# Kernel tuning notes

Hardware: AMD Instinct MI355X
Metric: run time of the kernel (lower is better)

## Reference

```python
import jax, jax.numpy as jnp
import numpy as np

HID = 64

def setup_inputs() -> dict:
    key = jax.random.key(0)
    ks = jax.random.split(key, 32)
    Nc, Na, B = 65536, 8192, 128
    Ecc, Eca, Eac, Eaa = 1048576, 262144, 262144, 131072
    d = {}
    d['x_context'] = jax.random.normal(ks[0], (Nc, 2), jnp.float32)
    d['x_action'] = jax.random.normal(ks[1], (Na, 2), jnp.float32)
    d['timestep'] = jax.random.randint(ks[2], (B,), 0, 1000)
    d['batch_idx'] = jax.random.randint(ks[3], (Na,), 0, B)
    d['cc_src'] = jax.random.randint(ks[4], (Ecc,), 0, Nc)
    d['cc_dst'] = jax.random.randint(ks[5], (Ecc,), 0, Nc)
    d['ca_src'] = jax.random.randint(ks[6], (Eca,), 0, Nc)
    d['ca_dst'] = jax.random.randint(ks[7], (Eca,), 0, Na)
    d['ac_src'] = jax.random.randint(ks[8], (Eac,), 0, Na)
    d['ac_dst'] = jax.random.randint(ks[9], (Eac,), 0, Nc)
    d['aa_src'] = jax.random.randint(ks[10], (Eaa,), 0, Na)
    d['aa_dst'] = jax.random.randint(ks[11], (Eaa,), 0, Na)
    def w(k, shape, fan_in):
        return jax.random.normal(k, shape, jnp.float32) / np.sqrt(fan_in)
    # input embeddings
    d['W_ctx'] = w(ks[12], (2, HID), 2); d['b_ctx'] = jnp.zeros((HID,), jnp.float32)
    d['W_act'] = w(ks[13], (2, HID), 2); d['b_act'] = jnp.zeros((HID,), jnp.float32)
    # time MLP
    d['tW1'] = w(ks[14], (HID, 2 * HID), HID); d['tb1'] = jnp.zeros((2 * HID,), jnp.float32)
    d['tW2'] = w(ks[15], (2 * HID, HID), 2 * HID); d['tb2'] = jnp.zeros((HID,), jnp.float32)
    # 2 SAGE layers, 4 edge types each (stacked: [cc, ca, ac, aa])
    d['c1_Wl'] = w(ks[16], (4, HID, HID), HID); d['c1_bl'] = jnp.zeros((4, HID), jnp.float32)
    d['c1_Wr'] = w(ks[17], (4, HID, HID), HID)
    d['c2_Wl'] = w(ks[18], (4, HID, HID), HID); d['c2_bl'] = jnp.zeros((4, HID), jnp.float32)
    d['c2_Wr'] = w(ks[19], (4, HID, HID), HID)
    # noise predictor
    d['nW1'] = w(ks[20], (2 * HID, HID), 2 * HID); d['nb1'] = jnp.zeros((HID,), jnp.float32)
    d['nW2'] = w(ks[21], (HID, 2), HID); d['nb2'] = jnp.zeros((2,), jnp.float32)
    return d


def _sage(x_src, x_dst, src, dst, Wl, bl, Wr):
    # PyG SAGEConv: lin_l(mean of neighbor msgs) + lin_r(self)
    n_dst = x_dst.shape[0]
    s = jax.ops.segment_sum(x_src[src], dst, num_segments=n_dst)
    cnt = jax.ops.segment_sum(jnp.ones((src.shape[0], 1), x_src.dtype), dst, num_segments=n_dst)
    mean = s / jnp.maximum(cnt, 1.0)
    return mean @ Wl + bl + x_dst @ Wr


def reference(x_context, x_action, timestep, batch_idx, cc_src, cc_dst, ca_src, ca_dst, ac_src, ac_dst, aa_src, aa_dst, W_ctx, b_ctx, W_act, b_act, tW1, tb1, tW2, tb2, c1_Wl, c1_bl, c1_Wr, c2_Wl, c2_bl, c2_Wr, nW1, nb1, nW2, nb2):
    h_ctx = x_context @ W_ctx + b_ctx           # [Nc, H]
    h_act = x_action @ W_act + b_act            # [Na, H]
    # hetero SAGE layer 1 (aggr='sum' over edge types per dst node type)
    o_ctx = (_sage(h_ctx, h_ctx, cc_src, cc_dst, c1_Wl[0], c1_bl[0], c1_Wr[0])
             + _sage(h_act, h_ctx, ac_src, ac_dst, c1_Wl[2], c1_bl[2], c1_Wr[2]))
    o_act = (_sage(h_ctx, h_act, ca_src, ca_dst, c1_Wl[1], c1_bl[1], c1_Wr[1])
             + _sage(h_act, h_act, aa_src, aa_dst, c1_Wl[3], c1_bl[3], c1_Wr[3]))
    h_ctx, h_act = jax.nn.relu(o_ctx), jax.nn.relu(o_act)
    # hetero SAGE layer 2
    o_act = (_sage(h_ctx, h_act, ca_src, ca_dst, c2_Wl[1], c2_bl[1], c2_Wr[1])
             + _sage(h_act, h_act, aa_src, aa_dst, c2_Wl[3], c2_bl[3], c2_Wr[3]))
    action_features = o_act                      # [Na, H]
    # sinusoidal time embedding + MLP
    half = HID // 2
    freqs = jnp.exp(-jnp.log(10000.0) * jnp.arange(half, dtype=jnp.float32) / (half - 1))
    ang = timestep.astype(jnp.float32)[:, None] * freqs[None, :]
    temb = jnp.concatenate([jnp.sin(ang), jnp.cos(ang)], axis=-1)   # [B, H]
    temb = jax.nn.gelu(temb @ tW1 + tb1, approximate=False) @ tW2 + tb2
    # gather per-node time embedding, fuse, predict noise
    fused = jnp.concatenate([action_features, temb[batch_idx]], axis=-1)  # [Na, 2H]
    h = jax.nn.gelu(fused @ nW1 + nb1, approximate=False)
    return h @ nW2 + nb2                         # [Na, node_features]
```

## Files before the change

### kernel.cpp

```cpp
#include <hip/hip_runtime.h>
#include <math.h>

#define HID 64
#define SLOTS 8192
#define WCC 32
#define WAC 10
#define SCA 8
#define SAA 4
#define HCA 16
#define HAA 8
#define CAP_CA 112
#define CAP_AA 80

__device__ __forceinline__ float gelu_exact(float x) {
    return 0.5f * x * (1.0f + erff(x * 0.70710678118654752f));
}

__device__ __forceinline__ float bf2f(unsigned short u) {
    return __uint_as_float(((unsigned int)u) << 16);
}
__device__ __forceinline__ unsigned short f2bf(float x) {
    unsigned int b = __float_as_uint(x);
    b += 0x7FFFu + ((b >> 16) & 1u);
    return (unsigned short)(b >> 16);
}

#define FXS 32768.0f
#define FXB (1 << 19)

__device__ __forceinline__ unsigned long long pack_edge(float2 v) {
    unsigned int f0 = (unsigned int)(__float2int_rn(v.x * FXS) + FXB);
    unsigned int f1 = (unsigned int)(__float2int_rn(v.y * FXS) + FXB);
    return (1ULL << 52) | ((unsigned long long)f1 << 26) | f0;
}

__device__ __forceinline__ void decode_acc(unsigned long long A, float& s0, float& s1, float& c) {
    int cnt = (int)(A >> 52);
    long long f0 = (long long)(A & 0x3FFFFFFULL) - (long long)cnt * FXB;
    long long f1 = (long long)((A >> 26) & 0x3FFFFFFULL) - (long long)cnt * FXB;
    s0 = (float)f0 * (1.0f / FXS);
    s1 = (float)f1 * (1.0f / FXS);
    c = (float)cnt;
}

__global__ __launch_bounds__(1024) void k1_kernel(
    const float* __restrict__ W_ctx, const float* __restrict__ b_ctx,
    const float* __restrict__ W_act, const float* __restrict__ b_act,
    const float* __restrict__ c1_Wl, const float* __restrict__ c1_bl,
    const float* __restrict__ c1_Wr,
    const float* __restrict__ c2_Wr, const float* __restrict__ c2_bl,
    float* __restrict__ P,
    const int* __restrict__ timestep,
    const float* __restrict__ tW1, const float* __restrict__ tb1,
    const float* __restrict__ tW2, const float* __restrict__ tb2,
    float* __restrict__ temb, int B,
    const int* __restrict__ cc_src, const int* __restrict__ cc_dst,
    const float* __restrict__ x_ctx, unsigned long long* __restrict__ pcc,
    int Ecc, int perCC,
    const int* __restrict__ ac_src, const int* __restrict__ ac_dst,
    const float* __restrict__ x_act, unsigned long long* __restrict__ pac,
    int Eac, int perAC,
    const int* __restrict__ ca_src, const int* __restrict__ ca_dst, int Eca,
    const int* __restrict__ aa_src, const int* __restrict__ aa_dst, int Eaa,
    unsigned long long* __restrict__ pca, unsigned long long* __restrict__ paa,
    int* __restrict__ hca, int* __restrict__ haa,
    int Nc, int bCC, int bAC, int bXA, int bXB, int bHA, int bHB) {
    __shared__ unsigned long long slab[SLOTS];
    int blk = blockIdx.x;
    int tid = threadIdx.x;

    if (blk < 6) {
        int m = blk;
        const float* vw = (m == 0 || m == 1 || m == 4) ? W_ctx : W_act;
        const float* vb = (m == 0 || m == 1 || m == 4) ? b_ctx : b_act;
        const float* L1; const float* L2 = nullptr; int off;
        if (m == 0)      { L1 = c1_Wr;            L2 = c1_Wr + 2 * 4096; off = 0; }
        else if (m == 1) { L1 = c1_Wl;                                   off = 192; }
        else if (m == 2) { L1 = c1_Wl + 2 * 4096;                        off = 384; }
        else if (m == 3) { L1 = c1_Wr + 4096;     L2 = c1_Wr + 3 * 4096; off = 576; }
        else if (m == 4) { L1 = c1_Wl + 4096;                            off = 768; }
        else             { L1 = c1_Wl + 3 * 4096;                        off = 960; }
        int j = tid & 63, kc = tid >> 6;
        float a0 = 0.f, a1 = 0.f, cc = 0.f;
        #pragma unroll
        for (int kk = 0; kk < 4; kk++) {
            int k = kc * 4 + kk;
            float l = L1[k * 64 + j];
            if (L2) l += L2[k * 64 + j];
            a0 += vw[k] * l; a1 += vw[64 + k] * l; cc += vb[k] * l;
        }
        float* red = (float*)slab;
        red[(kc * 3 + 0) * 64 + j] = a0;
        red[(kc * 3 + 1) * 64 + j] = a1;
        red[(kc * 3 + 2) * 64 + j] = cc;
        __syncthreads();
        if (tid < 192) {
            int row = tid >> 6, jj = tid & 63;
            float s = 0.f;
            #pragma unroll
            for (int q = 0; q < 16; q++) s += red[(q * 3 + row) * 64 + jj];
            if (row == 2) {
                if (m == 0) s += c1_bl[jj] + c1_bl[128 + jj];
                if (m == 3) s += c1_bl[64 + jj] + c1_bl[192 + jj];
            }
            P[off + row * 64 + jj] = s;
        }
    } else if (blk == 6) {
        const float4* A4 = (const float4*)(c2_Wr + 4096);
        const float4* B4 = (const float4*)(c2_Wr + 3 * 4096);
        float4* O4 = (float4*)(P + 1152);
        float4 a = A4[tid], b = B4[tid];
        O4[tid] = make_float4(a.x + b.x, a.y + b.y, a.z + b.z, a.w + b.w);
        if (tid < 64) P[5248 + tid] = c2_bl[64 + tid] + c2_bl[192 + tid];
    } else if (blk < bCC) {
        float* fl = (float*)slab;
        int sub = tid >> 7;
        int t = tid & 127;
        int b = (blk - 7) * 8 + sub;
        bool vb = (b < B);
        float* e = fl + sub * 64;
        float* t1 = fl + 2048 + sub * 128;
        float ts = vb ? (float)timestep[b] : 0.f;
        if (t < 64) {
            int jj = t & 31;
            float f = expf(-9.210340371976184f * (float)jj / 31.0f);
            float ang = ts * f;
            e[t] = (t < 32) ? sinf(ang) : cosf(ang);
        }
        __syncthreads();
        {
            float a = tb1[t];
            #pragma unroll 8
            for (int k = 0; k < 64; k++) a += e[k] * tW1[k * 128 + t];
            t1[t] = gelu_exact(a);
        }
        __syncthreads();
        if (t < 64 && vb) {
            float a = tb2[t];
            #pragma unroll 8
            for (int k = 0; k < 128; k++) a += t1[k] * tW2[k * 64 + t];
            temb[b * 64 + t] = a;
        }
    } else if (blk < bAC) {
        int q = blk - bCC;
        int r = q / WCC, s = q % WCC;
        for (int k = tid; k < SLOTS; k += 1024) slab[k] = 0;
        __syncthreads();
        int lo = r * SLOTS;
        int e0 = s * perCC;
        int e1 = min(e0 + perCC, Ecc);
        const float2* xc2 = (const float2*)x_ctx;
        for (int e = e0 + tid * 4; e < e1; e += 4096) {
            int4 d4 = *(const int4*)(cc_dst + e);
            unsigned int o0 = (unsigned int)(d4.x - lo);
            unsigned int o1 = (unsigned int)(d4.y - lo);
            unsigned int o2 = (unsigned int)(d4.z - lo);
            unsigned int o3 = (unsigned int)(d4.w - lo);
            if ((o0 < SLOTS) | (o1 < SLOTS) | (o2 < SLOTS) | (o3 < SLOTS)) {
                int4 s4 = *(const int4*)(cc_src + e);
                if (o0 < SLOTS) atomicAdd(&slab[o0], pack_edge(xc2[s4.x]));
                if (o1 < SLOTS) atomicAdd(&slab[o1], pack_edge(xc2[s4.y]));
                if (o2 < SLOTS) atomicAdd(&slab[o2], pack_edge(xc2[s4.z]));
                if (o3 < SLOTS) atomicAdd(&slab[o3], pack_edge(xc2[s4.w]));
            }
        }
        __syncthreads();
        for (int k = tid; k < SLOTS; k += 1024)
            pcc[(size_t)s * Nc + lo + k] = slab[k];
    } else if (blk < bXA) {
        int q = blk - bAC;
        int r = q / WAC, s = q % WAC;
        for (int k = tid; k < SLOTS; k += 1024) slab[k] = 0;
        __syncthreads();
        int lo = r * SLOTS;
        int e0 = s * perAC;
        int e1 = min(e0 + perAC, Eac);
        const float2* xa2 = (const float2*)x_act;
        for (int e = e0 + tid * 4; e < e1; e += 4096) {
            int4 d4 = *(const int4*)(ac_dst + e);
            unsigned int o0 = (unsigned int)(d4.x - lo);
            unsigned int o1 = (unsigned int)(d4.y - lo);
            unsigned int o2 = (unsigned int)(d4.z - lo);
            unsigned int o3 = (unsigned int)(d4.w - lo);
            if ((o0 < SLOTS) | (o1 < SLOTS) | (o2 < SLOTS) | (o3 < SLOTS)) {
                int4 s4 = *(const int4*)(ac_src + e);
                if (o0 < SLOTS) atomicAdd(&slab[o0], pack_edge(xa2[s4.x]));
                if (o1 < SLOTS) atomicAdd(&slab[o1], pack_edge(xa2[s4.y]));
                if (o2 < SLOTS) atomicAdd(&slab[o2], pack_edge(xa2[s4.z]));
                if (o3 < SLOTS) atomicAdd(&slab[o3], pack_edge(xa2[s4.w]));
            }
        }
        __syncthreads();
        for (int k = tid; k < SLOTS; k += 1024)
            pac[(size_t)s * Nc + lo + k] = slab[k];
    } else if (blk < bXB) {
        int s = blk - bXA;
        for (int k = tid; k < SLOTS; k += 1024) slab[k] = 0;
        __syncthreads();
        int per = (Eca + SCA - 1) / SCA;
        int e0 = s * per, e1 = min(e0 + per, Eca);
        const float2* xc2 = (const float2*)x_ctx;
        for (int e = e0 + tid * 4; e < e1; e += 4096) {
            int4 d4 = *(const int4*)(ca_dst + e);
            int4 s4 = *(const int4*)(ca_src + e);
            atomicAdd(&slab[d4.x], pack_edge(xc2[s4.x]));
            atomicAdd(&slab[d4.y], pack_edge(xc2[s4.y]));
            atomicAdd(&slab[d4.z], pack_edge(xc2[s4.z]));
            atomicAdd(&slab[d4.w], pack_edge(xc2[s4.w]));
        }
        __syncthreads();
        for (int k = tid; k < SLOTS; k += 1024)
            pca[(size_t)s * SLOTS + k] = slab[k];
    } else if (blk < bHA) {
        int s = blk - bXB;
        for (int k = tid; k < SLOTS; k += 1024) slab[k] = 0;
        __syncthreads();
        int per = (Eaa + SAA - 1) / SAA;
        int e0 = s * per, e1 = min(e0 + per, Eaa);
        const float2* xa2 = (const float2*)x_act;
        for (int e = e0 + tid * 4; e < e1; e += 4096) {
            int4 d4 = *(const int4*)(aa_dst + e);
            int4 s4 = *(const int4*)(aa_src + e);
            atomicAdd(&slab[d4.x], pack_edge(xa2[s4.x]));
            atomicAdd(&slab[d4.y], pack_edge(xa2[s4.y]));
            atomicAdd(&slab[d4.z], pack_edge(xa2[s4.z]));
            atomicAdd(&slab[d4.w], pack_edge(xa2[s4.w]));
        }
        __syncthreads();
        for (int k = tid; k < SLOTS; k += 1024)
            paa[(size_t)s * SLOTS + k] = slab[k];
    } else if (blk < bHB) {
        int s = blk - bHA;
        int* hist = (int*)slab;
        for (int k = tid; k < SLOTS; k += 1024) hist[k] = 0;
        __syncthreads();
        int per = (Eca + HCA - 1) / HCA;
        int e0 = s * per, e1 = min(e0 + per, Eca);
        for (int e = e0 + tid * 4; e < e1; e += 4096) {
            int4 d4 = *(const int4*)(ca_dst + e);
            atomicAdd(&hist[d4.x], 1); atomicAdd(&hist[d4.y], 1);
            atomicAdd(&hist[d4.z], 1); atomicAdd(&hist[d4.w], 1);
        }
        __syncthreads();
        for (int k = tid; k < SLOTS; k += 1024) hca[s * SLOTS + k] = hist[k];
    } else {
        int s = blk - bHB;
        int* hist = (int*)slab;
        for (int k = tid; k < SLOTS; k += 1024) hist[k] = 0;
        __syncthreads();
        int per = (Eaa + HAA - 1) / HAA;
        int e0 = s * per, e1 = min(e0 + per, Eaa);
        for (int e = e0 + tid * 4; e < e1; e += 4096) {
            int4 d4 = *(const int4*)(aa_dst + e);
            atomicAdd(&hist[d4.x], 1); atomicAdd(&hist[d4.y], 1);
            atomicAdd(&hist[d4.z], 1); atomicAdd(&hist[d4.w], 1);
        }
        __syncthreads();
        for (int k = tid; k < SLOTS; k += 1024) haa[s * SLOTS + k] = hist[k];
    }
}

__global__ void k2_kernel(int* __restrict__ hca, int* __restrict__ haa,
                          int* __restrict__ cnt_ca, int* __restrict__ cnt_aa) {
    int d = blockIdx.x * 1024 + threadIdx.x;
    int run = 0;
    #pragma unroll
    for (int s = 0; s < HCA; s++) {
        int h = hca[s * SLOTS + d];
        hca[s * SLOTS + d] = run;
        run += h;
    }
    cnt_ca[d] = run;
    run = 0;
    #pragma unroll
    for (int s = 0; s < HAA; s++) {
        int h = haa[s * SLOTS + d];
        haa[s * SLOTS + d] = run;
        run += h;
    }
    cnt_aa[d] = run;
}

__global__ __launch_bounds__(1024) void k3_kernel(
    const int* __restrict__ ca_src, const int* __restrict__ ca_dst, int Eca,
    const int* __restrict__ aa_src, const int* __restrict__ aa_dst, int Eaa,
    const int* __restrict__ hca, const int* __restrict__ haa,
    int* __restrict__ csr_ca, int* __restrict__ csr_aa,
    const unsigned long long* __restrict__ pcc, const unsigned long long* __restrict__ pac,
    const unsigned long long* __restrict__ pca, const unsigned long long* __restrict__ paa,
    const float* __restrict__ x_ctx, const float* __restrict__ x_act,
    const float* __restrict__ P,
    unsigned short* __restrict__ hb_ctx, unsigned short* __restrict__ hb_act,
    int Nc, int Na, int bCTX, int bACT) {
    __shared__ int sh[SLOTS];
    int blk = blockIdx.x;
    int tid = threadIdx.x;

    if (blk < HCA) {
        int s = blk;
        for (int k = tid; k < SLOTS; k += 1024) sh[k] = hca[s * SLOTS + k];
        __syncthreads();
        int per = (Eca + HCA - 1) / HCA;
        int e0 = s * per, e1 = min(e0 + per, Eca);
        for (int e = e0 + tid * 4; e < e1; e += 4096) {
            int4 d4 = *(const int4*)(ca_dst + e);
            int4 s4 = *(const int4*)(ca_src + e);
            int p0 = atomicAdd(&sh[d4.x], 1);
            int p1 = atomicAdd(&sh[d4.y], 1);
            int p2 = atomicAdd(&sh[d4.z], 1);
            int p3 = atomicAdd(&sh[d4.w], 1);
            if (p0 < CAP_CA) csr_ca[d4.x * CAP_CA + p0] = s4.x;
            if (p1 < CAP_CA) csr_ca[d4.y * CAP_CA + p1] = s4.y;
            if (p2 < CAP_CA) csr_ca[d4.z * CAP_CA + p2] = s4.z;
            if (p3 < CAP_CA) csr_ca[d4.w * CAP_CA + p3] = s4.w;
        }
    } else if (blk < bCTX) {
        int s = blk - HCA;
        for (int k = tid; k < SLOTS; k += 1024) sh[k] = haa[s * SLOTS + k];
        __syncthreads();
        int per = (Eaa + HAA - 1) / HAA;
        int e0 = s * per, e1 = min(e0 + per, Eaa);
        for (int e = e0 + tid * 4; e < e1; e += 4096) {
            int4 d4 = *(const int4*)(aa_dst + e);
            int4 s4 = *(const int4*)(aa_src + e);
            int p0 = atomicAdd(&sh[d4.x], 1);
            int p1 = atomicAdd(&sh[d4.y], 1);
            int p2 = atomicAdd(&sh[d4.z], 1);
            int p3 = atomicAdd(&sh[d4.w], 1);
            if (p0 < CAP_AA) csr_aa[d4.x * CAP_AA + p0] = s4.x;
            if (p1 < CAP_AA) csr_aa[d4.y * CAP_AA + p1] = s4.y;
            if (p2 < CAP_AA) csr_aa[d4.z * CAP_AA + p2] = s4.z;
            if (p3 < CAP_AA) csr_aa[d4.w * CAP_AA + p3] = s4.w;
        }
    } else if (blk < bACT) {
        float (*nd)[8] = (float(*)[8])sh;
        int i = (blk - bCTX) * 1024 + tid;
        if (i < Nc) {
            unsigned long long A = 0, Bv = 0;
            #pragma unroll 8
            for (int s = 0; s < WCC; s++) A += pcc[(size_t)s * Nc + i];
            #pragma unroll
            for (int s = 0; s < WAC; s++) Bv += pac[(size_t)s * Nc + i];
            float s0, s1, cc, a0, a1, ca;
            decode_acc(A, s0, s1, cc);
            decode_acc(Bv, a0, a1, ca);
            float2 xv = ((const float2*)x_ctx)[i];
            float rcc = 1.f / fmaxf(cc, 1.f), rac = 1.f / fmaxf(ca, 1.f);
            nd[tid][0] = s0 * rcc; nd[tid][1] = s1 * rcc; nd[tid][2] = (cc > 0.f) ? 1.f : 0.f;
            nd[tid][3] = a0 * rac; nd[tid][4] = a1 * rac; nd[tid][5] = (ca > 0.f) ? 1.f : 0.f;
            nd[tid][6] = xv.x; nd[tid][7] = xv.y;
        }
        __syncthreads();
        int ns = tid >> 6, j = tid & 63;
        float p0 = P[j], p1 = P[64 + j], p2 = P[128 + j];
        float p3 = P[192 + j], p4 = P[256 + j], p5 = P[320 + j];
        float p6 = P[384 + j], p7 = P[448 + j], p8 = P[512 + j];
        for (int it = 0; it < 64; it++) {
            int ln = it * 16 + ns;
            int gi = (blk - bCTX) * 1024 + ln;
            if (gi >= Nc) break;
            float o = nd[ln][6] * p0 + nd[ln][7] * p1 + p2
                    + nd[ln][0] * p3 + nd[ln][1] * p4 + nd[ln][2] * p5
                    + nd[ln][3] * p6 + nd[ln][4] * p7 + nd[ln][5] * p8;
            hb_ctx[(size_t)gi * 64 + j] = f2bf(fmaxf(o, 0.f));
        }
    } else {
        float (*nd)[8] = (float(*)[8])sh;
        int i = (blk - bACT) * 1024 + tid;
        if (i < Na) {
            unsigned long long A = 0, Bv = 0;
            #pragma unroll
            for (int s = 0; s < SCA; s++) A += pca[(size_t)s * SLOTS + i];
            #pragma unroll
            for (int s = 0; s < SAA; s++) Bv += paa[(size_t)s * SLOTS + i];
            float s0, s1, cc, a0, a1, ca;
            decode_acc(A, s0, s1, cc);
            decode_acc(Bv, a0, a1, ca);
            float2 xv = ((const float2*)x_act)[i];
            float rca = 1.f / fmaxf(cc, 1.f), raa = 1.f / fmaxf(ca, 1.f);
            nd[tid][0] = s0 * rca; nd[tid][1] = s1 * rca; nd[tid][2] = (cc > 0.f) ? 1.f : 0.f;
            nd[tid][3] = a0 * raa; nd[tid][4] = a1 * raa; nd[tid][5] = (ca > 0.f) ? 1.f : 0.f;
            nd[tid][6] = xv.x; nd[tid][7] = xv.y;
        }
        __syncthreads();
        int ns = tid >> 6, j = tid & 63;
        float p0 = P[576 + j], p1 = P[640 + j], p2 = P[704 + j];
        float p3 = P[768 + j], p4 = P[832 + j], p5 = P[896 + j];
        float p6 = P[960 + j], p7 = P[1024 + j], p8 = P[1088 + j];
        for (int it = 0; it < 64; it++) {
            int ln = it * 16 + ns;
            int gi = (blk - bACT) * 1024 + ln;
            if (gi >= Na) break;
            float o = nd[ln][6] * p0 + nd[ln][7] * p1 + p2
                    + nd[ln][0] * p3 + nd[ln][1] * p4 + nd[ln][2] * p5
                    + nd[ln][3] * p6 + nd[ln][4] * p7 + nd[ln][5] * p8;
            hb_act[(size_t)gi * 64 + j] = f2bf(fmaxf(o, 0.f));
        }
    }
}

__global__ void k4_kernel(const unsigned short* __restrict__ hb_ctx,
                          const unsigned short* __restrict__ hb_act,
                          const int* __restrict__ cnt_ca, const int* __restrict__ csr_ca,
                          const int* __restrict__ cnt_aa, const int* __restrict__ csr_aa,
                          const float* __restrict__ c2_Wl, const float* __restrict__ P,
                          const float* __restrict__ temb, const int* __restrict__ batch_idx,
                          const float* __restrict__ nW1, const float* __restrict__ nb1,
                          const float* __restrict__ nW2, const float* __restrict__ nb2,
                          float* __restrict__ out, int N) {
    int n = threadIdx.x >> 6;
    int l = threadIdx.x & 63;
    int half = l >> 5;
    int c2 = l & 31;
    int i = blockIdx.x * 4 + n;
    bool act = (i < N);
    __shared__ float smca[4][64], smaa[4][64], shr[4][64], sfused[4][128], sh1[4][64];

    const unsigned int* hc32 = (const unsigned int*)hb_ctx;
    const unsigned int* ha32 = (const unsigned int*)hb_act;

    if (act) {
        int m = cnt_ca[i], mi = min(m, CAP_CA);
        int b = i * CAP_CA;
        float s0 = 0.f, s1 = 0.f;
        #pragma unroll 4
        for (int k = half; k < mi; k += 2) {
            unsigned int w = hc32[(size_t)csr_ca[b + k] * 32 + c2];
            s0 += bf2f((unsigned short)(w & 0xFFFFu));
            s1 += bf2f((unsigned short)(w >> 16));
        }
        s0 += __shfl_xor(s0, 32);
        s1 += __shfl_xor(s1, 32);
        float rm = 1.f / fmaxf((float)m, 1.f);
        if (half == 0) { smca[n][c2 * 2] = s0 * rm; smca[n][c2 * 2 + 1] = s1 * rm; }

        m = cnt_aa[i]; mi = min(m, CAP_AA);
        b = i * CAP_AA;
        s0 = 0.f; s1 = 0.f;
        #pragma unroll 4
        for (int k = half; k < mi; k += 2) {
            unsigned int w = ha32[(size_t)csr_aa[b + k] * 32 + c2];
            s0 += bf2f((unsigned short)(w & 0xFFFFu));
            s1 += bf2f((unsigned short)(w >> 16));
        }
        s0 += __shfl_xor(s0, 32);
        s1 += __shfl_xor(s1, 32);
        rm = 1.f / fmaxf((float)m, 1.f);
        if (half == 0) { smaa[n][c2 * 2] = s0 * rm; smaa[n][c2 * 2 + 1] = s1 * rm; }

        shr[n][l] = bf2f(hb_act[(size_t)i * 64 + l]);
    }
    __syncthreads();

    if (act) {
        const float* Wl1  = c2_Wl + 4096;
        const float* Wl3  = c2_Wl + 3 * 4096;
        const float* Wr2s = P + 1152;
        float o = P[5248 + l];
        #pragma unroll 8
        for (int k = 0; k < 64; k++) {
            o += smca[n][k] * Wl1[k * 64 + l]
               + smaa[n][k] * Wl3[k * 64 + l]
               + shr[n][k]  * Wr2s[k * 64 + l];
        }
        sfused[n][l] = o;
        sfused[n][64 + l] = temb[(size_t)batch_idx[i] * 64 + l];
    }
    __syncthreads();

    if (act) {
        float h = nb1[l];
        #pragma unroll 8
        for (int k = 0; k < 128; k++) h += sfused[n][k] * nW1[k * 64 + l];
        sh1[n][l] = gelu_exact(h);
    }
    __syncthreads();

    if (act && l < 2) {
        float v = nb2[l];
        #pragma unroll 8
        for (int k = 0; k < 64; k++) v += sh1[n][k] * nW2[k * 2 + l];
        out[(size_t)i * 2 + l] = v;
    }
}

extern "C" void kernel_launch(void* const* d_in, const int* in_sizes, int n_in,
                              void* d_out, int out_size, void* d_ws, size_t ws_size,
                              hipStream_t stream) {
    const float* x_context = (const float*)d_in[0];
    const float* x_action  = (const float*)d_in[1];
    const int*   timestep  = (const int*)d_in[2];
    const int*   batch_idx = (const int*)d_in[3];
    const int*   cc_src = (const int*)d_in[4];
    const int*   cc_dst = (const int*)d_in[5];
    const int*   ca_src = (const int*)d_in[6];
    const int*   ca_dst = (const int*)d_in[7];
    const int*   ac_src = (const int*)d_in[8];
    const int*   ac_dst = (const int*)d_in[9];
    const int*   aa_src = (const int*)d_in[10];
    const int*   aa_dst = (const int*)d_in[11];
    const float* W_ctx = (const float*)d_in[12];
    const float* b_ctx = (const float*)d_in[13];
    const float* W_act = (const float*)d_in[14];
    const float* b_act = (const float*)d_in[15];
    const float* tW1 = (const float*)d_in[16];
    const float* tb1 = (const float*)d_in[17];
    const float* tW2 = (const float*)d_in[18];
    const float* tb2 = (const float*)d_in[19];
    const float* c1_Wl = (const float*)d_in[20];
    const float* c1_bl = (const float*)d_in[21];
    const float* c1_Wr = (const float*)d_in[22];
    const float* c2_Wl = (const float*)d_in[23];
    const float* c2_bl = (const float*)d_in[24];
    const float* c2_Wr = (const float*)d_in[25];
    const float* nW1 = (const float*)d_in[26];
    const float* nb1 = (const float*)d_in[27];
    const float* nW2 = (const float*)d_in[28];
    const float* nb2 = (const float*)d_in[29];
    float* out = (float*)d_out;

    const int Nc  = in_sizes[0] / 2;
    const int Na  = in_sizes[1] / 2;
    const int B   = in_sizes[2];
    const int Ecc = in_sizes[4];
    const int Eca = in_sizes[6];
    const int Eac = in_sizes[8];
    const int Eaa = in_sizes[10];

    char* ws = (char*)d_ws;
    size_t o = 0;
    unsigned long long* pcc = (unsigned long long*)(ws + o); o += (size_t)WCC * Nc * 8;
    unsigned long long* pac = (unsigned long long*)(ws + o); o += (size_t)WAC * Nc * 8;
    unsigned long long* pca = (unsigned long long*)(ws + o); o += (size_t)SCA * SLOTS * 8;
    unsigned long long* paa = (unsigned long long*)(ws + o); o += (size_t)SAA * SLOTS * 8;
    int* hca    = (int*)(ws + o); o += (size_t)HCA * SLOTS * 4;
    int* haa    = (int*)(ws + o); o += (size_t)HAA * SLOTS * 4;
    int* cnt_ca = (int*)(ws + o); o += (size_t)Na * 4;
    int* cnt_aa = (int*)(ws + o); o += (size_t)Na * 4;
    int* csr_ca = (int*)(ws + o); o += (size_t)Na * CAP_CA * 4;
    int* csr_aa = (int*)(ws + o); o += (size_t)Na * CAP_AA * 4;
    float* P    = (float*)(ws + o); o += 8192 * 4;
    float* temb = (float*)(ws + o); o += (size_t)B * 64 * 4;
    unsigned short* hb_ctx = (unsigned short*)(ws + o); o += (size_t)Nc * 64 * 2;
    unsigned short* hb_act = (unsigned short*)(ws + o); o += (size_t)Na * 64 * 2;
    if (o > ws_size) return;

    const int RNG = (Nc + SLOTS - 1) / SLOTS;
    const int nT  = (B + 7) / 8;
    const int bCC = 7 + nT;
    const int bAC = bCC + RNG * WCC;
    const int bXA = bAC + RNG * WAC;
    const int bXB = bXA + SCA;
    const int bHA = bXB + SAA;
    const int bHB = bHA + HCA;
    const int G1  = bHB + HAA;
    const int perCC = (((Ecc + WCC - 1) / WCC) + 3) & ~3;
    const int perAC = (((Eac + WAC - 1) / WAC) + 3) & ~3;

    k1_kernel<<<G1, 1024, 0, stream>>>(
        W_ctx, b_ctx, W_act, b_act, c1_Wl, c1_bl, c1_Wr, c2_Wr, c2_bl, P,
        timestep, tW1, tb1, tW2, tb2, temb, B,
        cc_src, cc_dst, x_context, pcc, Ecc, perCC,
        ac_src, ac_dst, x_action, pac, Eac, perAC,
        ca_src, ca_dst, Eca, aa_src, aa_dst, Eaa,
        pca, paa, hca, haa,
        Nc, bCC, bAC, bXA, bXB, bHA, bHB);

    k2_kernel<<<(Na + 1023) / 1024, 1024, 0, stream>>>(hca, haa, cnt_ca, cnt_aa);

    const int bCTX = HCA + HAA;
    const int GctxB = (Nc + 1023) / 1024;
    const int bACT = bCTX + GctxB;
    const int GactB = (Na + 1023) / 1024;
    k3_kernel<<<bACT + GactB, 1024, 0, stream>>>(
        ca_src, ca_dst, Eca, aa_src, aa_dst, Eaa,
        hca, haa, csr_ca, csr_aa,
        pcc, pac, pca, paa,
        x_context, x_action, P, hb_ctx, hb_act,
        Nc, Na, bCTX, bACT);

    k4_kernel<<<(Na + 3) / 4, 256, 0, stream>>>(
        hb_ctx, hb_act, cnt_ca, csr_ca, cnt_aa, csr_aa,
        c2_Wl, P, temb, batch_idx, nW1, nb1, nW2, nb2, out, Na);
}
```

Before: 100.4 us.

## Split fused multi-role kernels into separate per-stage launches

Breaks the block-index-dispatched kernel k1 into four kernels: weight precompute plus time MLP, cc scatter, ac scatter, and ca/aa scatter plus histograms. It likewise splits k3 into a CSR-fill kernel and a node-update kernel. Each kernel now declares only the shared memory it needs, so the small time-MLP blocks no longer reserve a 64KB slab. Independent stages that used to run concurrently inside one grid now run one after another on the stream, which adds launch gaps and removes that overlap.

After: 143.4 us. 1.43x slower.

```diff
diff --git a/kernel.cpp b/kernel.cpp
--- a/kernel.cpp
+++ b/kernel.cpp
@@ -43,7 +43,7 @@
     c = (float)cnt;
 }
 
-__global__ __launch_bounds__(1024) void k1_kernel(
+__global__ __launch_bounds__(1024) void kA_kernel(
     const float* __restrict__ W_ctx, const float* __restrict__ b_ctx,
     const float* __restrict__ W_act, const float* __restrict__ b_act,
     const float* __restrict__ c1_Wl, const float* __restrict__ c1_bl,
@@ -53,19 +53,8 @@
     const int* __restrict__ timestep,
     const float* __restrict__ tW1, const float* __restrict__ tb1,
     const float* __restrict__ tW2, const float* __restrict__ tb2,
-    float* __restrict__ temb, int B,
-    const int* __restrict__ cc_src, const int* __restrict__ cc_dst,
-    const float* __restrict__ x_ctx, unsigned long long* __restrict__ pcc,
-    int Ecc, int perCC,
-    const int* __restrict__ ac_src, const int* __restrict__ ac_dst,
-    const float* __restrict__ x_act, unsigned long long* __restrict__ pac,
-    int Eac, int perAC,
-    const int* __restrict__ ca_src, const int* __restrict__ ca_dst, int Eca,
-    const int* __restrict__ aa_src, const int* __restrict__ aa_dst, int Eaa,
-    unsigned long long* __restrict__ pca, unsigned long long* __restrict__ paa,
-    int* __restrict__ hca, int* __restrict__ haa,
-    int Nc, int bCC, int bAC, int bXA, int bXB, int bHA, int bHB) {
-    __shared__ unsigned long long slab[SLOTS];
+    float* __restrict__ temb, int B) {
+    __shared__ float fl[3072];
     int blk = blockIdx.x;
     int tid = threadIdx.x;
 
@@ -89,16 +78,15 @@
             if (L2) l += L2[k * 64 + j];
             a0 += vw[k] * l; a1 += vw[64 + k] * l; cc += vb[k] * l;
         }
-        float* red = (float*)slab;
-        red[(kc * 3 + 0) * 64 + j] = a0;
-        red[(kc * 3 + 1) * 64 + j] = a1;
-        red[(kc * 3 + 2) * 64 + j] = cc;
+        fl[(kc * 3 + 0) * 64 + j] = a0;
+        fl[(kc * 3 + 1) * 64 + j] = a1;
+        fl[(kc * 3 + 2) * 64 + j] = cc;
         __syncthreads();
         if (tid < 192) {
             int row = tid >> 6, jj = tid & 63;
             float s = 0.f;
             #pragma unroll
-            for (int q = 0; q < 16; q++) s += red[(q * 3 + row) * 64 + jj];
+            for (int q = 0; q < 16; q++) s += fl[(q * 3 + row) * 64 + jj];
             if (row == 2) {
                 if (m == 0) s += c1_bl[jj] + c1_bl[128 + jj];
                 if (m == 3) s += c1_bl[64 + jj] + c1_bl[192 + jj];
@@ -112,14 +100,13 @@
         float4 a = A4[tid], b = B4[tid];
         O4[tid] = make_float4(a.x + b.x, a.y + b.y, a.z + b.z, a.w + b.w);
         if (tid < 64) P[5248 + tid] = c2_bl[64 + tid] + c2_bl[192 + tid];
-    } else if (blk < bCC) {
-        float* fl = (float*)slab;
+    } else {
         int sub = tid >> 7;
         int t = tid & 127;
         int b = (blk - 7) * 8 + sub;
         bool vb = (b < B);
         float* e = fl + sub * 64;
-        float* t1 = fl + 2048 + sub * 128;
+        float* t1 = fl + 2048 + ((sub & 7) * 128);
         float ts = vb ? (float)timestep[b] : 0.f;
         if (t < 64) {
             int jj = t & 31;
@@ -132,69 +119,94 @@
             float a = tb1[t];
             #pragma unroll 8
             for (int k = 0; k < 64; k++) a += e[k] * tW1[k * 128 + t];
-            t1[t] = gelu_exact(a);
+            fl[1024 + sub * 128 + t] = gelu_exact(a);
         }
         __syncthreads();
         if (t < 64 && vb) {
+            const float* t1p = fl + 1024 + sub * 128;
             float a = tb2[t];
             #pragma unroll 8
-            for (int k = 0; k < 128; k++) a += t1[k] * tW2[k * 64 + t];
+            for (int k = 0; k < 128; k++) a += t1p[k] * tW2[k * 64 + t];
             temb[b * 64 + t] = a;
         }
-    } else if (blk < bAC) {
-        int q = blk - bCC;
-        int r = q / WCC, s = q % WCC;
-        for (int k = tid; k < SLOTS; k += 1024) slab[k] = 0;
-        __syncthreads();
-        int lo = r * SLOTS;
-        int e0 = s * perCC;
-        int e1 = min(e0 + perCC, Ecc);
-        const float2* xc2 = (const float2*)x_ctx;
-        for (int e = e0 + tid * 4; e < e1; e += 4096) {
-            int4 d4 = *(const int4*)(cc_dst + e);
-            unsigned int o0 = (unsigned int)(d4.x - lo);
-            unsigned int o1 = (unsigned int)(d4.y - lo);
-            unsigned int o2 = (unsigned int)(d4.z - lo);
-            unsigned int o3 = (unsigned int)(d4.w - lo);
-            if ((o0 < SLOTS) | (o1 < SLOTS) | (o2 < SLOTS) | (o3 < SLOTS)) {
-                int4 s4 = *(const int4*)(cc_src + e);
-                if (o0 < SLOTS) atomicAdd(&slab[o0], pack_edge(xc2[s4.x]));
-                if (o1 < SLOTS) atomicAdd(&slab[o1], pack_edge(xc2[s4.y]));
-                if (o2 < SLOTS) atomicAdd(&slab[o2], pack_edge(xc2[s4.z]));
-                if (o3 < SLOTS) atomicAdd(&slab[o3], pack_edge(xc2[s4.w]));
-            }
-        }
-        __syncthreads();
-        for (int k = tid; k < SLOTS; k += 1024)
-            pcc[(size_t)s * Nc + lo + k] = slab[k];
-    } else if (blk < bXA) {
-        int q = blk - bAC;
-        int r = q / WAC, s = q % WAC;
-        for (int k = tid; k < SLOTS; k += 1024) slab[k] = 0;
-        __syncthreads();
-        int lo = r * SLOTS;
-        int e0 = s * perAC;
-        int e1 = min(e0 + perAC, Eac);
-        const float2* xa2 = (const float2*)x_act;
-        for (int e = e0 + tid * 4; e < e1; e += 4096) {
-            int4 d4 = *(const int4*)(ac_dst + e);
-            unsigned int o0 = (unsigned int)(d4.x - lo);
-            unsigned int o1 = (unsigned int)(d4.y - lo);
-            unsigned int o2 = (unsigned int)(d4.z - lo);
-            unsigned int o3 = (unsigned int)(d4.w - lo);
-            if ((o0 < SLOTS) | (o1 < SLOTS) | (o2 < SLOTS) | (o3 < SLOTS)) {
-                int4 s4 = *(const int4*)(ac_src + e);
-                if (o0 < SLOTS) atomicAdd(&slab[o0], pack_edge(xa2[s4.x]));
-                if (o1 < SLOTS) atomicAdd(&slab[o1], pack_edge(xa2[s4.y]));
-                if (o2 < SLOTS) atomicAdd(&slab[o2], pack_edge(xa2[s4.z]));
-                if (o3 < SLOTS) atomicAdd(&slab[o3], pack_edge(xa2[s4.w]));
-            }
-        }
-        __syncthreads();
-        for (int k = tid; k < SLOTS; k += 1024)
-            pac[(size_t)s * Nc + lo + k] = slab[k];
-    } else if (blk < bXB) {
-        int s = blk - bXA;
+    }
+}
+
+__global__ __launch_bounds__(1024) void kB_kernel(
+    const int* __restrict__ cc_src, const int* __restrict__ cc_dst,
+    const float* __restrict__ x_ctx, unsigned long long* __restrict__ pcc,
+    int Ecc, int perCC, int Nc) {
+    __shared__ unsigned long long slab[SLOTS];
+    int tid = threadIdx.x;
+    int r = blockIdx.x / WCC, s = blockIdx.x % WCC;
+    for (int k = tid; k < SLOTS; k += 1024) slab[k] = 0;
+    __syncthreads();
+    int lo = r * SLOTS;
+    int e0 = s * perCC;
+    int e1 = min(e0 + perCC, Ecc);
+    const float2* xc2 = (const float2*)x_ctx;
+    for (int e = e0 + tid * 4; e < e1; e += 4096) {
+        int4 d4 = *(const int4*)(cc_dst + e);
+        unsigned int o0 = (unsigned int)(d4.x - lo);
+        unsigned int o1 = (unsigned int)(d4.y - lo);
+        unsigned int o2 = (unsigned int)(d4.z - lo);
+        unsigned int o3 = (unsigned int)(d4.w - lo);
+        if ((o0 < SLOTS) | (o1 < SLOTS) | (o2 < SLOTS) | (o3 < SLOTS)) {
+            int4 s4 = *(const int4*)(cc_src + e);
+            if (o0 < SLOTS) atomicAdd(&slab[o0], pack_edge(xc2[s4.x]));
+            if (o1 < SLOTS) atomicAdd(&slab[o1], pack_edge(xc2[s4.y]));
+            if (o2 < SLOTS) atomicAdd(&slab[o2], pack_edge(xc2[s4.z]));
+            if (o3 < SLOTS) atomicAdd(&slab[o3], pack_edge(xc2[s4.w]));
+        }
+    }
+    __syncthreads();
+    for (int k = tid; k < SLOTS; k += 1024)
+        pcc[(size_t)s * Nc + lo + k] = slab[k];
+}
+
+__global__ __launch_bounds__(1024) void kC_kernel(
+    const int* __restrict__ ac_src, const int* __restrict__ ac_dst,
+    const float* __restrict__ x_act, unsigned long long* __restrict__ pac,
+    int Eac, int perAC, int Nc) {
+    __shared__ unsigned long long slab[SLOTS];
+    int tid = threadIdx.x;
+    int r = blockIdx.x / WAC, s = blockIdx.x % WAC;
+    for (int k = tid; k < SLOTS; k += 1024) slab[k] = 0;
+    __syncthreads();
+    int lo = r * SLOTS;
+    int e0 = s * perAC;
+    int e1 = min(e0 + perAC, Eac);
+    const float2* xa2 = (const float2*)x_act;
+    for (int e = e0 + tid * 4; e < e1; e += 4096) {
+        int4 d4 = *(const int4*)(ac_dst + e);
+        unsigned int o0 = (unsigned int)(d4.x - lo);
+        unsigned int o1 = (unsigned int)(d4.y - lo);
+        unsigned int o2 = (unsigned int)(d4.z - lo);
+        unsigned int o3 = (unsigned int)(d4.w - lo);
+        if ((o0 < SLOTS) | (o1 < SLOTS) | (o2 < SLOTS) | (o3 < SLOTS)) {
+            int4 s4 = *(const int4*)(ac_src + e);
+            if (o0 < SLOTS) atomicAdd(&slab[o0], pack_edge(xa2[s4.x]));
+            if (o1 < SLOTS) atomicAdd(&slab[o1], pack_edge(xa2[s4.y]));
+            if (o2 < SLOTS) atomicAdd(&slab[o2], pack_edge(xa2[s4.z]));
+            if (o3 < SLOTS) atomicAdd(&slab[o3], pack_edge(xa2[s4.w]));
+        }
+    }
+    __syncthreads();
+    for (int k = tid; k < SLOTS; k += 1024)
+        pac[(size_t)s * Nc + lo + k] = slab[k];
+}
+
+__global__ __launch_bounds__(1024) void kD_kernel(
+    const int* __restrict__ ca_src, const int* __restrict__ ca_dst, int Eca,
+    const int* __restrict__ aa_src, const int* __restrict__ aa_dst, int Eaa,
+    const float* __restrict__ x_ctx, const float* __restrict__ x_act,
+    unsigned long long* __restrict__ pca, unsigned long long* __restrict__ paa,
+    int* __restrict__ hca, int* __restrict__ haa) {
+    __shared__ unsigned long long slab[SLOTS];
+    int blk = blockIdx.x;
+    int tid = threadIdx.x;
+    if (blk < SCA) {
+        int s = blk;
         for (int k = tid; k < SLOTS; k += 1024) slab[k] = 0;
         __syncthreads();
         int per = (Eca + SCA - 1) / SCA;
@@ -211,8 +223,8 @@
         __syncthreads();
         for (int k = tid; k < SLOTS; k += 1024)
             pca[(size_t)s * SLOTS + k] = slab[k];
-    } else if (blk < bHA) {
-        int s = blk - bXB;
+    } else if (blk < SCA + SAA) {
+        int s = blk - SCA;
         for (int k = tid; k < SLOTS; k += 1024) slab[k] = 0;
         __syncthreads();
         int per = (Eaa + SAA - 1) / SAA;
@@ -229,8 +241,8 @@
         __syncthreads();
         for (int k = tid; k < SLOTS; k += 1024)
             paa[(size_t)s * SLOTS + k] = slab[k];
-    } else if (blk < bHB) {
-        int s = blk - bHA;
+    } else if (blk < SCA + SAA + HCA) {
+        int s = blk - SCA - SAA;
         int* hist = (int*)slab;
         for (int k = tid; k < SLOTS; k += 1024) hist[k] = 0;
         __syncthreads();
@@ -244,7 +256,7 @@
         __syncthreads();
         for (int k = tid; k < SLOTS; k += 1024) hca[s * SLOTS + k] = hist[k];
     } else {
-        int s = blk - bHB;
+        int s = blk - SCA - SAA - HCA;
         int* hist = (int*)slab;
         for (int k = tid; k < SLOTS; k += 1024) hist[k] = 0;
         __syncthreads();
@@ -281,21 +293,14 @@
     cnt_aa[d] = run;
 }
 
-__global__ __launch_bounds__(1024) void k3_kernel(
+__global__ __launch_bounds__(1024) void kE_kernel(
     const int* __restrict__ ca_src, const int* __restrict__ ca_dst, int Eca,
     const int* __restrict__ aa_src, const int* __restrict__ aa_dst, int Eaa,
     const int* __restrict__ hca, const int* __restrict__ haa,
-    int* __restrict__ csr_ca, int* __restrict__ csr_aa,
-    const unsigned long long* __restrict__ pcc, const unsigned long long* __restrict__ pac,
-    const unsigned long long* __restrict__ pca, const unsigned long long* __restrict__ paa,
-    const float* __restrict__ x_ctx, const float* __restrict__ x_act,
-    const float* __restrict__ P,
-    unsigned short* __restrict__ hb_ctx, unsigned short* __restrict__ hb_act,
-    int Nc, int Na, int bCTX, int bACT) {
+    int* __restrict__ csr_ca, int* __restrict__ csr_aa) {
     __shared__ int sh[SLOTS];
     int blk = blockIdx.x;
     int tid = threadIdx.x;
-
     if (blk < HCA) {
         int s = blk;
         for (int k = tid; k < SLOTS; k += 1024) sh[k] = hca[s * SLOTS + k];
@@ -314,7 +319,7 @@
             if (p2 < CAP_CA) csr_ca[d4.z * CAP_CA + p2] = s4.z;
             if (p3 < CAP_CA) csr_ca[d4.w * CAP_CA + p3] = s4.w;
         }
-    } else if (blk < bCTX) {
+    } else {
         int s = blk - HCA;
         for (int k = tid; k < SLOTS; k += 1024) sh[k] = haa[s * SLOTS + k];
         __syncthreads();
@@ -332,9 +337,21 @@
             if (p2 < CAP_AA) csr_aa[d4.z * CAP_AA + p2] = s4.z;
             if (p3 < CAP_AA) csr_aa[d4.w * CAP_AA + p3] = s4.w;
         }
-    } else if (blk < bACT) {
-        float (*nd)[8] = (float(*)[8])sh;
-        int i = (blk - bCTX) * 1024 + tid;
+    }
+}
+
+__global__ __launch_bounds__(1024) void kF_kernel(
+    const unsigned long long* __restrict__ pcc, const unsigned long long* __restrict__ pac,
+    const unsigned long long* __restrict__ pca, const unsigned long long* __restrict__ paa,
+    const float* __restrict__ x_ctx, const float* __restrict__ x_act,
+    const float* __restrict__ P,
+    unsigned short* __restrict__ hb_ctx, unsigned short* __restrict__ hb_act,
+    int Nc, int Na, int bACT) {
+    __shared__ float nd[1024][8];
+    int blk = blockIdx.x;
+    int tid = threadIdx.x;
+    if (blk < bACT) {
+        int i = blk * 1024 + tid;
         if (i < Nc) {
             unsigned long long A = 0, Bv = 0;
             #pragma unroll 8
@@ -357,7 +374,7 @@
         float p6 = P[384 + j], p7 = P[448 + j], p8 = P[512 + j];
         for (int it = 0; it < 64; it++) {
             int ln = it * 16 + ns;
-            int gi = (blk - bCTX) * 1024 + ln;
+            int gi = blk * 1024 + ln;
             if (gi >= Nc) break;
             float o = nd[ln][6] * p0 + nd[ln][7] * p1 + p2
                     + nd[ln][0] * p3 + nd[ln][1] * p4 + nd[ln][2] * p5
@@ -365,7 +382,6 @@
             hb_ctx[(size_t)gi * 64 + j] = f2bf(fmaxf(o, 0.f));
         }
     } else {
-        float (*nd)[8] = (float(*)[8])sh;
         int i = (blk - bACT) * 1024 + tid;
         if (i < Na) {
             unsigned long long A = 0, Bv = 0;
@@ -547,37 +563,28 @@
 
     const int RNG = (Nc + SLOTS - 1) / SLOTS;
     const int nT  = (B + 7) / 8;
-    const int bCC = 7 + nT;
-    const int bAC = bCC + RNG * WCC;
-    const int bXA = bAC + RNG * WAC;
-    const int bXB = bXA + SCA;
-    const int bHA = bXB + SAA;
-    const int bHB = bHA + HCA;
-    const int G1  = bHB + HAA;
     const int perCC = (((Ecc + WCC - 1) / WCC) + 3) & ~3;
     const int perAC = (((Eac + WAC - 1) / WAC) + 3) & ~3;
 
-    k1_kernel<<<G1, 1024, 0, stream>>>(
+    kA_kernel<<<7 + nT, 1024, 0, stream>>>(
         W_ctx, b_ctx, W_act, b_act, c1_Wl, c1_bl, c1_Wr, c2_Wr, c2_bl, P,
-        timestep, tW1, tb1, tW2, tb2, temb, B,
-        cc_src, cc_dst, x_context, pcc, Ecc, perCC,
-        ac_src, ac_dst, x_action, pac, Eac, perAC,
+        timestep, tW1, tb1, tW2, tb2, temb, B);
+
+    kB_kernel<<<RNG * WCC, 1024, 0, stream>>>(cc_src, cc_dst, x_context, pcc, Ecc, perCC, Nc);
+    kC_kernel<<<RNG * WAC, 1024, 0, stream>>>(ac_src, ac_dst, x_action, pac, Eac, perAC, Nc);
+    kD_kernel<<<SCA + SAA + HCA + HAA, 1024, 0, stream>>>(
         ca_src, ca_dst, Eca, aa_src, aa_dst, Eaa,
-        pca, paa, hca, haa,
-        Nc, bCC, bAC, bXA, bXB, bHA, bHB);
+        x_context, x_action, pca, paa, hca, haa);
 
     k2_kernel<<<(Na + 1023) / 1024, 1024, 0, stream>>>(hca, haa, cnt_ca, cnt_aa);
 
-    const int bCTX = HCA + HAA;
+    kE_kernel<<<HCA + HAA, 1024, 0, stream>>>(
+        ca_src, ca_dst, Eca, aa_src, aa_dst, Eaa, hca, haa, csr_ca, csr_aa);
+
     const int GctxB = (Nc + 1023) / 1024;
-    const int bACT = bCTX + GctxB;
     const int GactB = (Na + 1023) / 1024;
-    k3_kernel<<<bACT + GactB, 1024, 0, stream>>>(
-        ca_src, ca_dst, Eca, aa_src, aa_dst, Eaa,
-        hca, haa, csr_ca, csr_aa,
-        pcc, pac, pca, paa,
-        x_context, x_action, P, hb_ctx, hb_act,
-        Nc, Na, bCTX, bACT);
+    kF_kernel<<<GctxB + GactB, 1024, 0, stream>>>(
+        pcc, pac, pca, paa, x_context, x_action, P, hb_ctx, hb_act, Nc, Na, GctxB);
 
     k4_kernel<<<(Na + 3) / 4, 256, 0, stream>>>(
         hb_ctx, hb_act, cnt_ca, csr_ca, cnt_aa, csr_aa,
```

## Use 32-bit packed LDS atomics, fewer scatter partitions, and batched gather loads

Applied to the files above, without the earlier changes.

Replaces the 64-bit fixed-point packed LDS atomics with two 32-bit atomics per edge, each packing a count and one 17-bit-scaled coordinate. Scatter partition counts for cc/ac drop from 32/10 to 16/6, which cuts partial-buffer writes and the reduction reads. The layer-2 CSR gather loops are unrolled by hand to issue 8 or 4 independent loads before accumulating. Risks include lower fixed-point precision and overflow of the 7-bit count or 25-bit field at high-degree nodes, plus twice as many atomic instructions per edge.

Measured after the change: 96.60 us. 1.04x faster.

```diff
diff --git a/kernel.cpp b/kernel.cpp
--- a/kernel.cpp
+++ b/kernel.cpp
@@ -3,8 +3,8 @@
 
 #define HID 64
 #define SLOTS 8192
-#define WCC 32
-#define WAC 10
+#define WCC 16
+#define WAC 6
 #define SCA 8
 #define SAA 4
 #define HCA 16
@@ -25,21 +25,16 @@
     return (unsigned short)(b >> 16);
 }
 
-#define FXS 32768.0f
-#define FXB (1 << 19)
-
-__device__ __forceinline__ unsigned long long pack_edge(float2 v) {
-    unsigned int f0 = (unsigned int)(__float2int_rn(v.x * FXS) + FXB);
-    unsigned int f1 = (unsigned int)(__float2int_rn(v.y * FXS) + FXB);
-    return (1ULL << 52) | ((unsigned long long)f1 << 26) | f0;
-}
-
-__device__ __forceinline__ void decode_acc(unsigned long long A, float& s0, float& s1, float& c) {
-    int cnt = (int)(A >> 52);
-    long long f0 = (long long)(A & 0x3FFFFFFULL) - (long long)cnt * FXB;
-    long long f1 = (long long)((A >> 26) & 0x3FFFFFFULL) - (long long)cnt * FXB;
-    s0 = (float)f0 * (1.0f / FXS);
-    s1 = (float)f1 * (1.0f / FXS);
+__device__ __forceinline__ unsigned int pack32(float x) {
+    return (1u << 25) | (unsigned int)(__float2int_rn(x * 16384.f) + 131072);
+}
+__device__ __forceinline__ void decode32(unsigned int lo, unsigned int hi,
+                                         float& s0, float& s1, float& c) {
+    unsigned int cnt = lo >> 25;
+    int f0 = (int)(lo & 0x1FFFFFFu) - (int)(cnt << 17);
+    int f1 = (int)(hi & 0x1FFFFFFu) - (int)((hi >> 25) << 17);
+    s0 = (float)f0 * (1.0f / 16384.f);
+    s1 = (float)f1 * (1.0f / 16384.f);
     c = (float)cnt;
 }
 
@@ -66,6 +61,8 @@
     int* __restrict__ hca, int* __restrict__ haa,
     int Nc, int bCC, int bAC, int bXA, int bXB, int bHA, int bHB) {
     __shared__ unsigned long long slab[SLOTS];
+    unsigned int* slab32 = (unsigned int*)slab;
+    float* fl = (float*)slab;
     int blk = blockIdx.x;
     int tid = threadIdx.x;
 
@@ -89,16 +86,15 @@
             if (L2) l += L2[k * 64 + j];
             a0 += vw[k] * l; a1 += vw[64 + k] * l; cc += vb[k] * l;
         }
-        float* red = (float*)slab;
-        red[(kc * 3 + 0) * 64 + j] = a0;
-        red[(kc * 3 + 1) * 64 + j] = a1;
-        red[(kc * 3 + 2) * 64 + j] = cc;
+        fl[(kc * 3 + 0) * 64 + j] = a0;
+        fl[(kc * 3 + 1) * 64 + j] = a1;
+        fl[(kc * 3 + 2) * 64 + j] = cc;
         __syncthreads();
         if (tid < 192) {
             int row = tid >> 6, jj = tid & 63;
             float s = 0.f;
             #pragma unroll
-            for (int q = 0; q < 16; q++) s += red[(q * 3 + row) * 64 + jj];
+            for (int q = 0; q < 16; q++) s += fl[(q * 3 + row) * 64 + jj];
             if (row == 2) {
                 if (m == 0) s += c1_bl[jj] + c1_bl[128 + jj];
                 if (m == 3) s += c1_bl[64 + jj] + c1_bl[192 + jj];
@@ -113,13 +109,11 @@
         O4[tid] = make_float4(a.x + b.x, a.y + b.y, a.z + b.z, a.w + b.w);
         if (tid < 64) P[5248 + tid] = c2_bl[64 + tid] + c2_bl[192 + tid];
     } else if (blk < bCC) {
-        float* fl = (float*)slab;
         int sub = tid >> 7;
         int t = tid & 127;
         int b = (blk - 7) * 8 + sub;
         bool vb = (b < B);
         float* e = fl + sub * 64;
-        float* t1 = fl + 2048 + sub * 128;
         float ts = vb ? (float)timestep[b] : 0.f;
         if (t < 64) {
             int jj = t & 31;
@@ -132,13 +126,14 @@
             float a = tb1[t];
             #pragma unroll 8
             for (int k = 0; k < 64; k++) a += e[k] * tW1[k * 128 + t];
-            t1[t] = gelu_exact(a);
+            fl[1024 + sub * 128 + t] = gelu_exact(a);
         }
         __syncthreads();
         if (t < 64 && vb) {
+            const float* t1p = fl + 1024 + sub * 128;
             float a = tb2[t];
             #pragma unroll 8
-            for (int k = 0; k < 128; k++) a += t1[k] * tW2[k * 64 + t];
+            for (int k = 0; k < 128; k++) a += t1p[k] * tW2[k * 64 + t];
             temb[b * 64 + t] = a;
         }
     } else if (blk < bAC) {
@@ -158,10 +153,14 @@
             unsigned int o3 = (unsigned int)(d4.w - lo);
             if ((o0 < SLOTS) | (o1 < SLOTS) | (o2 < SLOTS) | (o3 < SLOTS)) {
                 int4 s4 = *(const int4*)(cc_src + e);
-                if (o0 < SLOTS) atomicAdd(&slab[o0], pack_edge(xc2[s4.x]));
-                if (o1 < SLOTS) atomicAdd(&slab[o1], pack_edge(xc2[s4.y]));
-                if (o2 < SLOTS) atomicAdd(&slab[o2], pack_edge(xc2[s4.z]));
-                if (o3 < SLOTS) atomicAdd(&slab[o3], pack_edge(xc2[s4.w]));
+                if (o0 < SLOTS) { float2 v = xc2[s4.x];
+                    atomicAdd(&slab32[2 * o0], pack32(v.x)); atomicAdd(&slab32[2 * o0 + 1], pack32(v.y)); }
+                if (o1 < SLOTS) { float2 v = xc2[s4.y];
+                    atomicAdd(&slab32[2 * o1], pack32(v.x)); atomicAdd(&slab32[2 * o1 + 1], pack32(v.y)); }
+                if (o2 < SLOTS) { float2 v = xc2[s4.z];
+                    atomicAdd(&slab32[2 * o2], pack32(v.x)); atomicAdd(&slab32[2 * o2 + 1], pack32(v.y)); }
+                if (o3 < SLOTS) { float2 v = xc2[s4.w];
+                    atomicAdd(&slab32[2 * o3], pack32(v.x)); atomicAdd(&slab32[2 * o3 + 1], pack32(v.y)); }
             }
         }
         __syncthreads();
@@ -184,10 +183,14 @@
             unsigned int o3 = (unsigned int)(d4.w - lo);
             if ((o0 < SLOTS) | (o1 < SLOTS) | (o2 < SLOTS) | (o3 < SLOTS)) {
                 int4 s4 = *(const int4*)(ac_src + e);
-                if (o0 < SLOTS) atomicAdd(&slab[o0], pack_edge(xa2[s4.x]));
-                if (o1 < SLOTS) atomicAdd(&slab[o1], pack_edge(xa2[s4.y]));
-                if (o2 < SLOTS) atomicAdd(&slab[o2], pack_edge(xa2[s4.z]));
-                if (o3 < SLOTS) atomicAdd(&slab[o3], pack_edge(xa2[s4.w]));
+                if (o0 < SLOTS) { float2 v = xa2[s4.x];
+                    atomicAdd(&slab32[2 * o0], pack32(v.x)); atomicAdd(&slab32[2 * o0 + 1], pack32(v.y)); }
+                if (o1 < SLOTS) { float2 v = xa2[s4.y];
+                    atomicAdd(&slab32[2 * o1], pack32(v.x)); atomicAdd(&slab32[2 * o1 + 1], pack32(v.y)); }
+                if (o2 < SLOTS) { float2 v = xa2[s4.z];
+                    atomicAdd(&slab32[2 * o2], pack32(v.x)); atomicAdd(&slab32[2 * o2 + 1], pack32(v.y)); }
+                if (o3 < SLOTS) { float2 v = xa2[s4.w];
+                    atomicAdd(&slab32[2 * o3], pack32(v.x)); atomicAdd(&slab32[2 * o3 + 1], pack32(v.y)); }
             }
         }
         __syncthreads();
@@ -203,10 +206,11 @@
         for (int e = e0 + tid * 4; e < e1; e += 4096) {
             int4 d4 = *(const int4*)(ca_dst + e);
             int4 s4 = *(const int4*)(ca_src + e);
-            atomicAdd(&slab[d4.x], pack_edge(xc2[s4.x]));
-            atomicAdd(&slab[d4.y], pack_edge(xc2[s4.y]));
-            atomicAdd(&slab[d4.z], pack_edge(xc2[s4.z]));
-            atomicAdd(&slab[d4.w], pack_edge(xc2[s4.w]));
+            float2 v0 = xc2[s4.x], v1 = xc2[s4.y], v2 = xc2[s4.z], v3 = xc2[s4.w];
+            atomicAdd(&slab32[2 * d4.x], pack32(v0.x)); atomicAdd(&slab32[2 * d4.x + 1], pack32(v0.y));
+            atomicAdd(&slab32[2 * d4.y], pack32(v1.x)); atomicAdd(&slab32[2 * d4.y + 1], pack32(v1.y));
+            atomicAdd(&slab32[2 * d4.z], pack32(v2.x)); atomicAdd(&slab32[2 * d4.z + 1], pack32(v2.y));
+            atomicAdd(&slab32[2 * d4.w], pack32(v3.x)); atomicAdd(&slab32[2 * d4.w + 1], pack32(v3.y));
         }
         __syncthreads();
         for (int k = tid; k < SLOTS; k += 1024)
@@ -221,10 +225,11 @@
         for (int e = e0 + tid * 4; e < e1; e += 4096) {
             int4 d4 = *(const int4*)(aa_dst + e);
             int4 s4 = *(const int4*)(aa_src + e);
-            atomicAdd(&slab[d4.x], pack_edge(xa2[s4.x]));
-            atomicAdd(&slab[d4.y], pack_edge(xa2[s4.y]));
-            atomicAdd(&slab[d4.z], pack_edge(xa2[s4.z]));
-            atomicAdd(&slab[d4.w], pack_edge(xa2[s4.w]));
+            float2 v0 = xa2[s4.x], v1 = xa2[s4.y], v2 = xa2[s4.z], v3 = xa2[s4.w];
+            atomicAdd(&slab32[2 * d4.x], pack32(v0.x)); atomicAdd(&slab32[2 * d4.x + 1], pack32(v0.y));
+            atomicAdd(&slab32[2 * d4.y], pack32(v1.x)); atomicAdd(&slab32[2 * d4.y + 1], pack32(v1.y));
+            atomicAdd(&slab32[2 * d4.z], pack32(v2.x)); atomicAdd(&slab32[2 * d4.z + 1], pack32(v2.y));
+            atomicAdd(&slab32[2 * d4.w], pack32(v3.x)); atomicAdd(&slab32[2 * d4.w + 1], pack32(v3.y));
         }
         __syncthreads();
         for (int k = tid; k < SLOTS; k += 1024)
@@ -336,14 +341,20 @@
         float (*nd)[8] = (float(*)[8])sh;
         int i = (blk - bCTX) * 1024 + tid;
         if (i < Nc) {
-            unsigned long long A = 0, Bv = 0;
+            unsigned int lo0 = 0, hi0 = 0, lo1 = 0, hi1 = 0;
             #pragma unroll 8
-            for (int s = 0; s < WCC; s++) A += pcc[(size_t)s * Nc + i];
+            for (int s = 0; s < WCC; s++) {
+                unsigned long long A = pcc[(size_t)s * Nc + i];
+                lo0 += (unsigned int)A; hi0 += (unsigned int)(A >> 32);
+            }
             #pragma unroll
-            for (int s = 0; s < WAC; s++) Bv += pac[(size_t)s * Nc + i];
+            for (int s = 0; s < WAC; s++) {
+                unsigned long long A = pac[(size_t)s * Nc + i];
+                lo1 += (unsigned int)A; hi1 += (unsigned int)(A >> 32);
+            }
             float s0, s1, cc, a0, a1, ca;
-            decode_acc(A, s0, s1, cc);
-            decode_acc(Bv, a0, a1, ca);
+            decode32(lo0, hi0, s0, s1, cc);
+            decode32(lo1, hi1, a0, a1, ca);
             float2 xv = ((const float2*)x_ctx)[i];
             float rcc = 1.f / fmaxf(cc, 1.f), rac = 1.f / fmaxf(ca, 1.f);
             nd[tid][0] = s0 * rcc; nd[tid][1] = s1 * rcc; nd[tid][2] = (cc > 0.f) ? 1.f : 0.f;
@@ -368,14 +379,20 @@
         float (*nd)[8] = (float(*)[8])sh;
         int i = (blk - bACT) * 1024 + tid;
         if (i < Na) {
-            unsigned long long A = 0, Bv = 0;
+            unsigned int lo0 = 0, hi0 = 0, lo1 = 0, hi1 = 0;
             #pragma unroll
-            for (int s = 0; s < SCA; s++) A += pca[(size_t)s * SLOTS + i];
+            for (int s = 0; s < SCA; s++) {
+                unsigned long long A = pca[(size_t)s * SLOTS + i];
+                lo0 += (unsigned int)A; hi0 += (unsigned int)(A >> 32);
+            }
             #pragma unroll
-            for (int s = 0; s < SAA; s++) Bv += paa[(size_t)s * SLOTS + i];
+            for (int s = 0; s < SAA; s++) {
+                unsigned long long A = paa[(size_t)s * SLOTS + i];
+                lo1 += (unsigned int)A; hi1 += (unsigned int)(A >> 32);
+            }
             float s0, s1, cc, a0, a1, ca;
-            decode_acc(A, s0, s1, cc);
-            decode_acc(Bv, a0, a1, ca);
+            decode32(lo0, hi0, s0, s1, cc);
+            decode32(lo1, hi1, a0, a1, ca);
             float2 xv = ((const float2*)x_act)[i];
             float rca = 1.f / fmaxf(cc, 1.f), raa = 1.f / fmaxf(ca, 1.f);
             nd[tid][0] = s0 * rca; nd[tid][1] = s1 * rca; nd[tid][2] = (cc > 0.f) ? 1.f : 0.f;
@@ -423,8 +440,20 @@
         int m = cnt_ca[i], mi = min(m, CAP_CA);
         int b = i * CAP_CA;
         float s0 = 0.f, s1 = 0.f;
-        #pragma unroll 4
-        for (int k = half; k < mi; k += 2) {
+        int k = half;
+        for (; k + 14 < mi; k += 16) {
+            int i0 = csr_ca[b + k], i1 = csr_ca[b + k + 2], i2 = csr_ca[b + k + 4], i3 = csr_ca[b + k + 6];
+            int i4 = csr_ca[b + k + 8], i5 = csr_ca[b + k + 10], i6 = csr_ca[b + k + 12], i7 = csr_ca[b + k + 14];
+            unsigned int w0 = hc32[(size_t)i0 * 32 + c2], w1 = hc32[(size_t)i1 * 32 + c2];
+            unsigned int w2 = hc32[(size_t)i2 * 32 + c2], w3 = hc32[(size_t)i3 * 32 + c2];
+            unsigned int w4 = hc32[(size_t)i4 * 32 + c2], w5 = hc32[(size_t)i5 * 32 + c2];
+            unsigned int w6 = hc32[(size_t)i6 * 32 + c2], w7 = hc32[(size_t)i7 * 32 + c2];
+            s0 += bf2f((unsigned short)w0) + bf2f((unsigned short)w1) + bf2f((unsigned short)w2) + bf2f((unsigned short)w3)
+                + bf2f((unsigned short)w4) + bf2f((unsigned short)w5) + bf2f((unsigned short)w6) + bf2f((unsigned short)w7);
+            s1 += bf2f((unsigned short)(w0 >> 16)) + bf2f((unsigned short)(w1 >> 16)) + bf2f((unsigned short)(w2 >> 16)) + bf2f((unsigned short)(w3 >> 16))
+                + bf2f((unsigned short)(w4 >> 16)) + bf2f((unsigned short)(w5 >> 16)) + bf2f((unsigned short)(w6 >> 16)) + bf2f((unsigned short)(w7 >> 16));
+        }
+        for (; k < mi; k += 2) {
             unsigned int w = hc32[(size_t)csr_ca[b + k] * 32 + c2];
             s0 += bf2f((unsigned short)(w & 0xFFFFu));
             s1 += bf2f((unsigned short)(w >> 16));
@@ -437,8 +466,15 @@
         m = cnt_aa[i]; mi = min(m, CAP_AA);
         b = i * CAP_AA;
         s0 = 0.f; s1 = 0.f;
-        #pragma unroll 4
-        for (int k = half; k < mi; k += 2) {
+        k = half;
+        for (; k + 6 < mi; k += 8) {
+            int i0 = csr_aa[b + k], i1 = csr_aa[b + k + 2], i2 = csr_aa[b + k + 4], i3 = csr_aa[b + k + 6];
+            unsigned int w0 = ha32[(size_t)i0 * 32 + c2], w1 = ha32[(size_t)i1 * 32 + c2];
+            unsigned int w2 = ha32[(size_t)i2 * 32 + c2], w3 = ha32[(size_t)i3 * 32 + c2];
+            s0 += bf2f((unsigned short)w0) + bf2f((unsigned short)w1) + bf2f((unsigned short)w2) + bf2f((unsigned short)w3);
+            s1 += bf2f((unsigned short)(w0 >> 16)) + bf2f((unsigned short)(w1 >> 16)) + bf2f((unsigned short)(w2 >> 16)) + bf2f((unsigned short)(w3 >> 16));
+        }
+        for (; k < mi; k += 2) {
             unsigned int w = ha32[(size_t)csr_aa[b + k] * 32 + c2];
             s0 += bf2f((unsigned short)(w & 0xFFFFu));
             s1 += bf2f((unsigned short)(w >> 16));
```
